# Optimization experiments

Hardware: AMD Instinct MI355X
Metric: run time of the kernel (lower is better)

Reference implementation:

```python
import jax, jax.numpy as jnp
import numpy as np

TEMPERATURE = 0.02
EPS = 1e-10
TOPK = 10


def setup_inputs() -> dict:
    key = jax.random.key(0)
    k1, k2 = jax.random.split(key)
    B = 8192
    sim_matrix = jax.random.normal(k1, (B, B), dtype=jnp.float32)
    pids = jax.random.randint(k2, (B,), 0, 1000, dtype=jnp.int64)
    return {"sim_matrix": sim_matrix, "pids": pids}


def reference(sim_matrix, pids):
    B = sim_matrix.shape[0]
    k = min(TOPK, B)

    # Entropy of the T->I matching distribution per row (matches torch exactly:
    # softmax over dim=1, then -sum p*log(p+eps)).
    probs = jax.nn.softmax(sim_matrix / TEMPERATURE, axis=1)  # [B, B]
    entropy = -jnp.sum(probs * jnp.log(probs + EPS), axis=1)  # [B]
    max_entropy = np.float32(np.log(B + EPS))
    normalized_entropy = entropy / max_entropy  # [B]

    # Vectorized top-k rank agreement between T->I rows and I->T rows
    # (replaces the original per-sample Python loop with set intersection;
    # top-k indices are unique, so counting pairwise equality == |set A & set B|).
    _, top_t2i = jax.lax.top_k(sim_matrix, k)      # [B, k]
    _, top_i2t = jax.lax.top_k(sim_matrix.T, k)    # [B, k]
    overlap = jnp.sum(
        top_t2i[:, :, None] == top_i2t[:, None, :], axis=(1, 2)
    )  # [B]
    rank_agreement = overlap.astype(sim_matrix.dtype) / k  # [B]

    uncertainty = (1.0 - rank_agreement) * 0.5 + normalized_entropy * 0.5
    return uncertainty, normalized_entropy
```

## Files before the change

### kernel.cpp

```cpp
#include <hip/hip_runtime.h>
#include <hip/hip_bf16.h>
#include <math.h>

constexpr int BB = 8192;
constexpr float INV_MAX_ENT = 1.0f / 9.010913347279288f;

__global__ __launch_bounds__(256) void rows_kernel(const float* __restrict__ sim,
                                                   float* __restrict__ out,
                                                   int* __restrict__ row_top) {
  const int row = blockIdx.x;
  const int t = threadIdx.x;
  const int lane = t & 63;
  const int wid = t >> 6;

  const float4* __restrict__ r4 =
      reinterpret_cast<const float4*>(sim + (size_t)row * BB);

  float x[32];
#pragma unroll
  for (int i4 = 0; i4 < 8; ++i4) {
    float4 v = r4[t + (i4 << 8)];
    x[i4 * 4 + 0] = v.x;
    x[i4 * 4 + 1] = v.y;
    x[i4 * 4 + 2] = v.z;
    x[i4 * 4 + 3] = v.w;
  }

  float m = x[0];
#pragma unroll
  for (int i = 1; i < 32; ++i) m = fmaxf(m, x[i]);
#pragma unroll
  for (int off = 32; off > 0; off >>= 1) m = fmaxf(m, __shfl_xor(m, off));
  __shared__ float smax[4];
  if (lane == 0) smax[wid] = m;
  __syncthreads();
  m = fmaxf(fmaxf(smax[0], smax[1]), fmaxf(smax[2], smax[3]));

  const float tm = 50.0f * m;
  float S = 0.0f, W = 0.0f;
#pragma unroll
  for (int i = 0; i < 32; ++i) {
    float d = fmaf(50.0f, x[i], -tm);
    float e = __expf(d);
    S += e;
    W += e * d;
  }
#pragma unroll
  for (int off = 32; off > 0; off >>= 1) {
    S += __shfl_xor(S, off);
    W += __shfl_xor(W, off);
  }
  __shared__ float sS[4], sW[4];
  if (lane == 0) { sS[wid] = S; sW[wid] = W; }
  __syncthreads();
  S = sS[0] + sS[1] + sS[2] + sS[3];
  W = sW[0] + sW[1] + sW[2] + sW[3];
  if (t == 0) {
    float ent = __logf(S) - W / S;
    out[BB + row] = ent * INV_MAX_ENT;
  }

  __shared__ float swv[4];
  __shared__ int swc[4];
#pragma unroll 1
  for (int kk = 0; kk < 10; ++kk) {
    float bv = x[0];
    int bc = (t << 2);
#pragma unroll
    for (int i4 = 0; i4 < 8; ++i4) {
#pragma unroll
      for (int j = 0; j < 4; ++j) {
        float v = x[i4 * 4 + j];
        int cc = (i4 << 10) + (t << 2) + j;
        if (v > bv) { bv = v; bc = cc; }
      }
    }
#pragma unroll
    for (int off = 32; off > 0; off >>= 1) {
      float ov = __shfl_xor(bv, off);
      int oc = __shfl_xor(bc, off);
      if (ov > bv || (ov == bv && oc < bc)) { bv = ov; bc = oc; }
    }
    if (lane == 0) { swv[wid] = bv; swc[wid] = bc; }
    __syncthreads();
    float fv = swv[0];
    int fc = swc[0];
#pragma unroll
    for (int w = 1; w < 4; ++w) {
      if (swv[w] > fv || (swv[w] == fv && swc[w] < fc)) { fv = swv[w]; fc = swc[w]; }
    }
    if (((fc >> 2) & 255) == t) {
      int li = ((fc >> 10) << 2) | (fc & 3);
#pragma unroll
      for (int i = 0; i < 32; ++i)
        if (i == li) x[i] = -INFINITY;
    }
    if (t == 0) row_top[kk * BB + row] = fc;
    __syncthreads();
  }
}

#define CAS_STEP(tvk, tik)                                  \
  if (v > tvk) {                                            \
    float _fv = tvk; tvk = v; v = _fv;                      \
    int _fi = tik; tik = id; id = _fi;                      \
  }

#define INS10(vv, ii)                                       \
  if ((vv) > tv9) {                                         \
    float v = (vv);                                         \
    int id = (ii);                                          \
    CAS_STEP(tv0, ti0) CAS_STEP(tv1, ti1)                   \
    CAS_STEP(tv2, ti2) CAS_STEP(tv3, ti3)                   \
    CAS_STEP(tv4, ti4) CAS_STEP(tv5, ti5)                   \
    CAS_STEP(tv6, ti6) CAS_STEP(tv7, ti7)                   \
    CAS_STEP(tv8, ti8) CAS_STEP(tv9, ti9)                   \
  }

#define DECL10                                              \
  float tv0 = -INFINITY, tv1 = -INFINITY, tv2 = -INFINITY,  \
        tv3 = -INFINITY, tv4 = -INFINITY, tv5 = -INFINITY,  \
        tv6 = -INFINITY, tv7 = -INFINITY, tv8 = -INFINITY,  \
        tv9 = -INFINITY;                                    \
  int ti0 = -1, ti1 = -1, ti2 = -1, ti3 = -1, ti4 = -1,     \
      ti5 = -1, ti6 = -1, ti7 = -1, ti8 = -1, ti9 = -1;

__global__ __launch_bounds__(256) void cols_partial_kernel(const float* __restrict__ sim,
                                                           float* __restrict__ pv,
                                                           int* __restrict__ pi,
                                                           int CH) {
  const int col = blockIdx.x * 256 + threadIdx.x;
  const int r0 = blockIdx.y * CH;

  DECL10;

  const float* __restrict__ p = sim + (size_t)r0 * BB + col;

  for (int rr = 0; rr < CH; rr += 4) {
    float v0 = p[0];
    float v1 = p[BB];
    float v2 = p[2 * BB];
    float v3 = p[3 * BB];
    p += (size_t)4 * BB;
    INS10(v0, r0 + rr + 0);
    INS10(v1, r0 + rr + 1);
    INS10(v2, r0 + rr + 2);
    INS10(v3, r0 + rr + 3);
  }

  float* __restrict__ pvb = pv + (size_t)blockIdx.y * 10 * BB + col;
  int* __restrict__ pib = pi + (size_t)blockIdx.y * 10 * BB + col;
  pvb[0 * BB] = tv0;  pib[0 * BB] = ti0;
  pvb[1 * BB] = tv1;  pib[1 * BB] = ti1;
  pvb[2 * BB] = tv2;  pib[2 * BB] = ti2;
  pvb[3 * BB] = tv3;  pib[3 * BB] = ti3;
  pvb[4 * BB] = tv4;  pib[4 * BB] = ti4;
  pvb[5 * BB] = tv5;  pib[5 * BB] = ti5;
  pvb[6 * BB] = tv6;  pib[6 * BB] = ti6;
  pvb[7 * BB] = tv7;  pib[7 * BB] = ti7;
  pvb[8 * BB] = tv8;  pib[8 * BB] = ti8;
  pvb[9 * BB] = tv9;  pib[9 * BB] = ti9;
}

__global__ __launch_bounds__(256) void merge_kernel(const float* __restrict__ pv,
                                                    const int* __restrict__ pi,
                                                    const int* __restrict__ row_top,
                                                    float* __restrict__ out,
                                                    int nch) {
  const int c = blockIdx.x * 256 + threadIdx.x;

  DECL10;

  for (int ch = 0; ch < nch; ++ch) {
    const float* __restrict__ pvb = pv + (size_t)ch * 10 * BB + c;
    const int* __restrict__ pib = pi + (size_t)ch * 10 * BB + c;
#pragma unroll
    for (int j = 0; j < 10; ++j) {
      float vj = pvb[j * BB];
      if (!(vj > tv9)) break;
      int idj = pib[j * BB];
      INS10(vj, idj);
    }
  }

  int cnt = 0;
#pragma unroll
  for (int kk = 0; kk < 10; ++kk) {
    int rt = row_top[kk * BB + c];
    cnt += (rt == ti0) + (rt == ti1) + (rt == ti2) + (rt == ti3) + (rt == ti4) +
           (rt == ti5) + (rt == ti6) + (rt == ti7) + (rt == ti8) + (rt == ti9);
  }
  float ne = out[BB + c];
  float ra = (float)cnt * 0.1f;
  out[c] = (1.0f - ra) * 0.5f + 0.5f * ne;
}

extern "C" void kernel_launch(void* const* d_in, const int* in_sizes, int n_in,
                              void* d_out, int out_size, void* d_ws, size_t ws_size,
                              hipStream_t stream) {
  const float* sim = (const float*)d_in[0];
  float* out = (float*)d_out;

  int nch = 32;
  while (nch > 1) {
    size_t need = (size_t)BB * 10 * 4 + (size_t)nch * BB * 10 * 8;
    if (need <= ws_size) break;
    nch >>= 1;
  }
  int* row_top = (int*)d_ws;
  float* pv = (float*)((char*)d_ws + (size_t)BB * 10 * 4);
  int* pi = (int*)((char*)pv + (size_t)nch * BB * 10 * 4);

  rows_kernel<<<BB, 256, 0, stream>>>(sim, out, row_top);
  dim3 gb(BB / 256, nch);
  cols_partial_kernel<<<gb, 256, 0, stream>>>(sim, pv, pi, BB / nch);
  merge_kernel<<<BB / 256, 256, 0, stream>>>(pv, pi, row_top, out, nch);
}
```

Baseline: 572.3 us.

## Use one wave per row with online softmax-entropy and per-lane top-10 merge

```diff
diff --git a/kernel.cpp b/kernel.cpp
--- a/kernel.cpp
+++ b/kernel.cpp
@@ -5,111 +5,16 @@
 constexpr int BB = 8192;
 constexpr float INV_MAX_ENT = 1.0f / 9.010913347279288f;
 
-__global__ __launch_bounds__(256) void rows_kernel(const float* __restrict__ sim,
-                                                   float* __restrict__ out,
-                                                   int* __restrict__ row_top) {
-  const int row = blockIdx.x;
-  const int t = threadIdx.x;
-  const int lane = t & 63;
-  const int wid = t >> 6;
-
-  const float4* __restrict__ r4 =
-      reinterpret_cast<const float4*>(sim + (size_t)row * BB);
-
-  float x[32];
-#pragma unroll
-  for (int i4 = 0; i4 < 8; ++i4) {
-    float4 v = r4[t + (i4 << 8)];
-    x[i4 * 4 + 0] = v.x;
-    x[i4 * 4 + 1] = v.y;
-    x[i4 * 4 + 2] = v.z;
-    x[i4 * 4 + 3] = v.w;
-  }
-
-  float m = x[0];
-#pragma unroll
-  for (int i = 1; i < 32; ++i) m = fmaxf(m, x[i]);
-#pragma unroll
-  for (int off = 32; off > 0; off >>= 1) m = fmaxf(m, __shfl_xor(m, off));
-  __shared__ float smax[4];
-  if (lane == 0) smax[wid] = m;
-  __syncthreads();
-  m = fmaxf(fmaxf(smax[0], smax[1]), fmaxf(smax[2], smax[3]));
-
-  const float tm = 50.0f * m;
-  float S = 0.0f, W = 0.0f;
-#pragma unroll
-  for (int i = 0; i < 32; ++i) {
-    float d = fmaf(50.0f, x[i], -tm);
-    float e = __expf(d);
-    S += e;
-    W += e * d;
-  }
-#pragma unroll
-  for (int off = 32; off > 0; off >>= 1) {
-    S += __shfl_xor(S, off);
-    W += __shfl_xor(W, off);
-  }
-  __shared__ float sS[4], sW[4];
-  if (lane == 0) { sS[wid] = S; sW[wid] = W; }
-  __syncthreads();
-  S = sS[0] + sS[1] + sS[2] + sS[3];
-  W = sW[0] + sW[1] + sW[2] + sW[3];
-  if (t == 0) {
-    float ent = __logf(S) - W / S;
-    out[BB + row] = ent * INV_MAX_ENT;
-  }
-
-  __shared__ float swv[4];
-  __shared__ int swc[4];
-#pragma unroll 1
-  for (int kk = 0; kk < 10; ++kk) {
-    float bv = x[0];
-    int bc = (t << 2);
-#pragma unroll
-    for (int i4 = 0; i4 < 8; ++i4) {
-#pragma unroll
-      for (int j = 0; j < 4; ++j) {
-        float v = x[i4 * 4 + j];
-        int cc = (i4 << 10) + (t << 2) + j;
-        if (v > bv) { bv = v; bc = cc; }
-      }
-    }
-#pragma unroll
-    for (int off = 32; off > 0; off >>= 1) {
-      float ov = __shfl_xor(bv, off);
-      int oc = __shfl_xor(bc, off);
-      if (ov > bv || (ov == bv && oc < bc)) { bv = ov; bc = oc; }
-    }
-    if (lane == 0) { swv[wid] = bv; swc[wid] = bc; }
-    __syncthreads();
-    float fv = swv[0];
-    int fc = swc[0];
-#pragma unroll
-    for (int w = 1; w < 4; ++w) {
-      if (swv[w] > fv || (swv[w] == fv && swc[w] < fc)) { fv = swv[w]; fc = swc[w]; }
-    }
-    if (((fc >> 2) & 255) == t) {
-      int li = ((fc >> 10) << 2) | (fc & 3);
-#pragma unroll
-      for (int i = 0; i < 32; ++i)
-        if (i == li) x[i] = -INFINITY;
-    }
-    if (t == 0) row_top[kk * BB + row] = fc;
-    __syncthreads();
-  }
-}
-
 #define CAS_STEP(tvk, tik)                                  \
-  if (v > tvk) {                                            \
-    float _fv = tvk; tvk = v; v = _fv;                      \
-    int _fi = tik; tik = id; id = _fi;                      \
+  if (_cv > tvk) {                                          \
+    float _fv = tvk; tvk = _cv; _cv = _fv;                  \
+    int _fi = tik; tik = _ci; _ci = _fi;                    \
   }
 
 #define INS10(vv, ii)                                       \
   if ((vv) > tv9) {                                         \
-    float v = (vv);                                         \
-    int id = (ii);                                          \
+    float _cv = (vv);                                       \
+    int _ci = (ii);                                         \
     CAS_STEP(tv0, ti0) CAS_STEP(tv1, ti1)                   \
     CAS_STEP(tv2, ti2) CAS_STEP(tv3, ti3)                   \
     CAS_STEP(tv4, ti4) CAS_STEP(tv5, ti5)                   \
@@ -125,6 +30,82 @@
   int ti0 = -1, ti1 = -1, ti2 = -1, ti3 = -1, ti4 = -1,     \
       ti5 = -1, ti6 = -1, ti7 = -1, ti8 = -1, ti9 = -1;
 
+#define POP_HEAD                                            \
+  tv0 = tv1; ti0 = ti1; tv1 = tv2; ti1 = ti2;               \
+  tv2 = tv3; ti2 = ti3; tv3 = tv4; ti3 = ti4;               \
+  tv4 = tv5; ti4 = ti5; tv5 = tv6; ti5 = ti6;               \
+  tv6 = tv7; ti6 = ti7; tv7 = tv8; ti7 = ti8;               \
+  tv8 = tv9; ti8 = ti9; tv9 = -INFINITY; ti9 = -1;
+
+__global__ __launch_bounds__(256) void rows_kernel(const float* __restrict__ sim,
+                                                   float* __restrict__ out,
+                                                   int* __restrict__ row_top) {
+  const int lane = threadIdx.x & 63;
+  const int wid = threadIdx.x >> 6;
+  const int row = blockIdx.x * 4 + wid;
+
+  const float4* __restrict__ r4 =
+      reinterpret_cast<const float4*>(sim + (size_t)row * BB);
+
+  DECL10;
+  float m = -1e30f, S = 0.0f, W = 0.0f;
+
+#pragma unroll 4
+  for (int j4 = 0; j4 < 32; ++j4) {
+    const int f = lane + (j4 << 6);
+    float4 q = r4[f];
+
+    float mx4 = fmaxf(fmaxf(q.x, q.y), fmaxf(q.z, q.w));
+    if (mx4 > tv9) {
+      const int base = f << 2;
+      INS10(q.x, base + 0);
+      INS10(q.y, base + 1);
+      INS10(q.z, base + 2);
+      INS10(q.w, base + 3);
+    }
+
+    float t0 = 50.0f * q.x, t1 = 50.0f * q.y, t2 = 50.0f * q.z, t3 = 50.0f * q.w;
+    float bm = fmaxf(fmaxf(t0, t1), fmaxf(t2, t3));
+    float mn = fmaxf(m, bm);
+    float r = __expf(m - mn);
+    float d0 = t0 - mn, d1 = t1 - mn, d2 = t2 - mn, d3 = t3 - mn;
+    float e0 = __expf(d0), e1 = __expf(d1), e2 = __expf(d2), e3 = __expf(d3);
+    W = fmaf(m - mn, S, W) * r + (d0 * e0 + d1 * e1 + d2 * e2 + d3 * e3);
+    S = fmaf(S, r, (e0 + e1) + (e2 + e3));
+    m = mn;
+  }
+
+#pragma unroll
+  for (int off = 32; off; off >>= 1) {
+    float m2 = __shfl_xor(m, off);
+    float S2 = __shfl_xor(S, off);
+    float W2 = __shfl_xor(W, off);
+    float mn = fmaxf(m, m2);
+    float ra = __expf(m - mn);
+    float rb = __expf(m2 - mn);
+    W = fmaf(m - mn, S, W) * ra + fmaf(m2 - mn, S2, W2) * rb;
+    S = S * ra + S2 * rb;
+    m = mn;
+  }
+  if (lane == 0) {
+    out[BB + row] = (__logf(S) - W / S) * INV_MAX_ENT;
+  }
+
+#pragma unroll 1
+  for (int kk = 0; kk < 10; ++kk) {
+    float v = tv0;
+    int i = ti0;
+#pragma unroll
+    for (int off = 32; off; off >>= 1) {
+      float ov = __shfl_xor(v, off);
+      int oi = __shfl_xor(i, off);
+      if (ov > v || (ov == v && oi < i)) { v = ov; i = oi; }
+    }
+    if (lane == 0) row_top[kk * BB + row] = i;
+    if (ti0 == i) { POP_HEAD }
+  }
+}
+
 __global__ __launch_bounds__(256) void cols_partial_kernel(const float* __restrict__ sim,
                                                            float* __restrict__ pv,
                                                            int* __restrict__ pi,
@@ -136,16 +117,28 @@
 
   const float* __restrict__ p = sim + (size_t)r0 * BB + col;
 
-  for (int rr = 0; rr < CH; rr += 4) {
-    float v0 = p[0];
-    float v1 = p[BB];
+  for (int rr = 0; rr < CH; rr += 8) {
+    float v0 = p[0 * BB];
+    float v1 = p[1 * BB];
     float v2 = p[2 * BB];
     float v3 = p[3 * BB];
-    p += (size_t)4 * BB;
-    INS10(v0, r0 + rr + 0);
-    INS10(v1, r0 + rr + 1);
-    INS10(v2, r0 + rr + 2);
-    INS10(v3, r0 + rr + 3);
+    float v4 = p[4 * BB];
+    float v5 = p[5 * BB];
+    float v6 = p[6 * BB];
+    float v7 = p[7 * BB];
+    p += (size_t)8 * BB;
+    float mx = fmaxf(fmaxf(fmaxf(v0, v1), fmaxf(v2, v3)),
+                     fmaxf(fmaxf(v4, v5), fmaxf(v6, v7)));
+    if (mx > tv9) {
+      INS10(v0, r0 + rr + 0);
+      INS10(v1, r0 + rr + 1);
+      INS10(v2, r0 + rr + 2);
+      INS10(v3, r0 + rr + 3);
+      INS10(v4, r0 + rr + 4);
+      INS10(v5, r0 + rr + 5);
+      INS10(v6, r0 + rr + 6);
+      INS10(v7, r0 + rr + 7);
+    }
   }
 
   float* __restrict__ pvb = pv + (size_t)blockIdx.y * 10 * BB + col;
@@ -201,7 +194,7 @@
   const float* sim = (const float*)d_in[0];
   float* out = (float*)d_out;
 
-  int nch = 32;
+  int nch = 64;
   while (nch > 1) {
     size_t need = (size_t)BB * 10 * 4 + (size_t)nch * BB * 10 * 8;
     if (need <= ws_size) break;
@@ -211,7 +204,7 @@
   float* pv = (float*)((char*)d_ws + (size_t)BB * 10 * 4);
   int* pi = (int*)((char*)pv + (size_t)nch * BB * 10 * 4);
 
-  rows_kernel<<<BB, 256, 0, stream>>>(sim, out, row_top);
+  rows_kernel<<<BB / 4, 256, 0, stream>>>(sim, out, row_top);
   dim3 gb(BB / 256, nch);
   cols_partial_kernel<<<gb, 256, 0, stream>>>(sim, pv, pi, BB / nch);
   merge_kernel<<<BB / 256, 256, 0, stream>>>(pv, pi, row_top, out, nch);
```

New measurement: 656.9 us. +14.8%, slower.
